# Kernel optimization log

Measured on AMD Instinct MI355X. Metric: run time of the kernel, lower is better.

## Reference

```python
import jax, jax.numpy as jnp
import numpy as np

B, L, D, DIN, S, R, K = 2, 1024, 1024, 2048, 16, 64, 4


def setup_inputs() -> dict:
    key = jax.random.key(0)
    ks = jax.random.split(key, 8)
    f = lambda k, sh, sc: jax.random.normal(k, sh, jnp.float32) * sc
    return {
        "x": f(ks[0], (B, L, D), 1.0),
        "norm_w": jnp.ones((D,), jnp.float32),
        "W_in": f(ks[1], (D, 2 * DIN), D ** -0.5),
        "conv_w": f(ks[2], (DIN, 1, K), 0.5),
        "conv_b": jnp.zeros((DIN,), jnp.float32),
        "W_x": f(ks[3], (DIN, R + 2 * S), DIN ** -0.5),
        "W_dt": f(ks[4], (R, DIN), R ** -0.5),
        "b_dt": f(ks[5], (DIN,), 0.1),
        "A_log": jnp.log(jnp.broadcast_to(jnp.arange(1, S + 1, dtype=jnp.float32), (DIN, S))),
        "D_skip": jnp.ones((DIN,), jnp.float32),
        "W_out": f(ks[6], (DIN, D), DIN ** -0.5),
    }


def reference(x, norm_w, W_in, conv_w, conv_b, W_x, W_dt, b_dt, A_log, D_skip, W_out):
    eps = 1e-5
    # RMSNorm
    xn = x * jax.lax.rsqrt(jnp.mean(x * x, axis=-1, keepdims=True) + eps) * norm_w
    # input projection -> (x_branch, gate)
    xz = xn @ W_in                       # [B,L,2*DIN]
    xi, z = jnp.split(xz, 2, axis=-1)
    # causal depthwise conv1d along L
    xt = jnp.transpose(xi, (0, 2, 1))    # [B,DIN,L]
    xc = jax.lax.conv_general_dilated(xt, conv_w, (1,), [(K - 1, 0)],
                                      feature_group_count=DIN)
    xc = jnp.transpose(xc, (0, 2, 1)) + conv_b
    xc = jax.nn.silu(xc)                 # [B,L,DIN]
    # input-dependent SSM parameters
    xd = xc @ W_x                        # [B,L,R+2S]
    dt, Bm, Cm = jnp.split(xd, [R, R + S], axis=-1)
    dt = jax.nn.softplus(dt @ W_dt + b_dt)           # [B,L,DIN]
    A = -jnp.exp(A_log)                              # [DIN,S]
    dA = jnp.exp(dt[..., None] * A)                  # [B,L,DIN,S]
    dBu = (dt * xc)[..., None] * Bm[:, :, None, :]   # [B,L,DIN,S]
    # selective scan: h_t = dA_t * h_{t-1} + dBu_t (parallel associative scan)
    def comb(c1, c2):
        a1, b1 = c1
        a2, b2 = c2
        return a1 * a2, a2 * b1 + b2
    _, h = jax.lax.associative_scan(comb, (dA, dBu), axis=1)
    y = jnp.einsum('blds,bls->bld', h, Cm) + D_skip * xc
    y = y * jax.nn.silu(z)
    return x + y @ W_out
```

## Files before the change

kernel.cpp:

```cpp
#include <hip/hip_runtime.h>

#define B_    2
#define L_    1024
#define D_    1024
#define DIN_  2048
#define S_    16
#define R_    64
#define NTOK  (B_ * L_)
#define NCH   32
#define LC    (L_ / NCH)

typedef unsigned short u16;
typedef short bf16x8 __attribute__((ext_vector_type(8)));
typedef float f32x4  __attribute__((ext_vector_type(4)));

__device__ __forceinline__ u16 f2bf(float f) {
    union { float f; unsigned u; } v; v.f = f;
    return (u16)((v.u + 0x7FFFu + ((v.u >> 16) & 1u)) >> 16);
}
__device__ __forceinline__ float bf2f(u16 b) {
    union { unsigned u; float f; } v; v.u = (unsigned)b << 16;
    return v.f;
}

__device__ __forceinline__ void transp_tile(
    const float* __restrict__ src, u16* __restrict__ dst,
    int R, int Csrc, int cx, int cy, int tx, int ty) {
    __shared__ float tile[32][33];
    int c0 = cx * 32, r0 = cy * 32;
#pragma unroll
    for (int i = 0; i < 32; i += 8)
        tile[ty + i][tx] = (c0 + tx < Csrc)
            ? src[(size_t)(r0 + ty + i) * Csrc + c0 + tx] : 0.f;
    __syncthreads();
#pragma unroll
    for (int i = 0; i < 32; i += 8)
        dst[(size_t)(c0 + ty + i) * R + r0 + tx] = f2bf(tile[tx][ty + i]);
}

__global__ __launch_bounds__(256) void prep_kernel(
    const float* __restrict__ x, const float* __restrict__ nw, u16* __restrict__ xn,
    const float* __restrict__ W_in,  u16* __restrict__ WinT,
    const float* __restrict__ W_out, u16* __restrict__ WoutT,
    const float* __restrict__ W_x,   u16* __restrict__ WxT,
    const float* __restrict__ W_dt,  u16* __restrict__ WdtT) {
    int bid = blockIdx.x;
    if (bid < NTOK) {
        int row = bid;
        const float4 v = ((const float4*)(x + (size_t)row * D_))[threadIdx.x];
        float ss = v.x * v.x + v.y * v.y + v.z * v.z + v.w * v.w;
#pragma unroll
        for (int o = 32; o > 0; o >>= 1) ss += __shfl_down(ss, o);
        __shared__ float red[4];
        if ((threadIdx.x & 63) == 0) red[threadIdx.x >> 6] = ss;
        __syncthreads();
        float tot = red[0] + red[1] + red[2] + red[3];
        float sc = rsqrtf(tot * (1.f / (float)D_) + 1e-5f);
        const float4 wv = ((const float4*)nw)[threadIdx.x];
        ushort4 o;
        o.x = f2bf(v.x * sc * wv.x);
        o.y = f2bf(v.y * sc * wv.y);
        o.z = f2bf(v.z * sc * wv.z);
        o.w = f2bf(v.w * sc * wv.w);
        ((ushort4*)(xn + (size_t)row * D_))[threadIdx.x] = o;
        return;
    }
    int b2 = bid - NTOK;
    int tx = threadIdx.x & 31, ty = threadIdx.x >> 5;
    if (b2 < 4096) {
        transp_tile(W_in, WinT, D_, 2 * DIN_, b2 % 128, b2 / 128, tx, ty);
    } else if (b2 < 6144) {
        int b = b2 - 4096;
        transp_tile(W_out, WoutT, DIN_, D_, b % 32, b / 32, tx, ty);
    } else if (b2 < 6400) {
        int b = b2 - 6144;
        transp_tile(W_x, WxT, DIN_, 96, b % 4, b / 4, tx, ty);
    } else {
        int b = b2 - 6400;
        transp_tile(W_dt, WdtT, R_, DIN_, b % 64, b / 64, tx, ty);
    }
}

#define BK 32
template<int BM, int BN, int CX>
__global__ __launch_bounds__(256) void gemm_bf16(
    const u16* __restrict__ A, int lda,
    const u16* __restrict__ Bt, int ldb,
    float* __restrict__ C, u16* __restrict__ Cbf, int ldc,
    const float* __restrict__ aux,
    int M, int N, int K, int mode) {
    constexpr int WGM = (BM >= 128) ? 2 : 1;
    constexpr int WGN = 4 / WGM;
    constexpr int FM = BM / (16 * WGM);
    constexpr int FN = BN / (16 * WGN);
    constexpr int ABYTES = BM * BK * 2;
    constexpr int BBYTES = BN * BK * 2;
    __shared__ __align__(16) u16 As[2][BM * BK];
    __shared__ __align__(16) u16 Bs[2][BN * BK];
    const int t = threadIdx.x;
    const int w = t >> 6;
    const int l = t & 63;
    const int lr = l & 15;
    const int kg = l >> 4;
    const int wm = (w / WGN) * (BM / WGM);
    const int wn = (w % WGN) * (BN / WGN);

    const int GX = gridDim.x, GY = gridDim.y;
    int h = blockIdx.x + GX * (blockIdx.y + GY * blockIdx.z);
    int xcd = h & 7, pos = h >> 3;
    int ncx = GX / CX;
    int chunk = (GX * GY * gridDim.z) >> 3;
    int rpc = chunk / CX;
    int bx = (xcd % ncx) * CX + pos % CX;
    int r  = (xcd / ncx) * rpc + pos / CX;
    int by = r % GY;
    int bz = r / GY;

    const int row0 = by * BM;
    const int col0 = bx * BN;
    const int kbase = bz * K;

    auto stage = [&](int buf, int k0) {
#pragma unroll
        for (int i = 0; i < ABYTES; i += 4096) {
            int off = i + t * 16;
            int grow = off >> 6;
            int sw = ((off >> 4) & 3) ^ ((grow >> 1) & 3);
            const u16* ga = A + (size_t)(row0 + grow) * lda + k0 + sw * 8;
            __builtin_amdgcn_global_load_lds(
                (const __attribute__((address_space(1))) unsigned int*)(const void*)ga,
                (__attribute__((address_space(3))) unsigned int*)(void*)&As[buf][off >> 1],
                16, 0, 0);
        }
#pragma unroll
        for (int i = 0; i < BBYTES; i += 4096) {
            int off = i + t * 16;
            int grow = off >> 6;
            int sw = ((off >> 4) & 3) ^ ((grow >> 1) & 3);
            const u16* gb = Bt + (size_t)(col0 + grow) * ldb + k0 + sw * 8;
            __builtin_amdgcn_global_load_lds(
                (const __attribute__((address_space(1))) unsigned int*)(const void*)gb,
                (__attribute__((address_space(3))) unsigned int*)(void*)&Bs[buf][off >> 1],
                16, 0, 0);
        }
    };

    f32x4 acc[FM][FN];
#pragma unroll
    for (int i = 0; i < FM; ++i)
#pragma unroll
        for (int j = 0; j < FN; ++j) acc[i][j] = (f32x4){0.f, 0.f, 0.f, 0.f};

    const int nt = K / BK;
    stage(0, kbase);
    asm volatile("s_waitcnt vmcnt(0)" ::: "memory");
    __builtin_amdgcn_s_barrier();
    asm volatile("" ::: "memory");

    int cur = 0;
    for (int tt = 0; tt < nt; ++tt) {
        if (tt + 1 < nt) stage(cur ^ 1, kbase + (tt + 1) * BK);
        bf16x8 af[FM], bfr[FN];
#pragma unroll
        for (int mt = 0; mt < FM; ++mt) {
            int ar = wm + mt * 16 + lr;
            af[mt] = *(const bf16x8*)&As[cur][ar * 32 + (kg ^ ((ar >> 1) & 3)) * 8];
        }
#pragma unroll
        for (int nt2 = 0; nt2 < FN; ++nt2) {
            int br = wn + nt2 * 16 + lr;
            bfr[nt2] = *(const bf16x8*)&Bs[cur][br * 32 + (kg ^ ((br >> 1) & 3)) * 8];
        }
        __builtin_amdgcn_s_setprio(1);
#pragma unroll
        for (int mt = 0; mt < FM; ++mt)
#pragma unroll
            for (int nt2 = 0; nt2 < FN; ++nt2)
                acc[mt][nt2] = __builtin_amdgcn_mfma_f32_16x16x32_bf16(
                    af[mt], bfr[nt2], acc[mt][nt2], 0, 0, 0);
        __builtin_amdgcn_s_setprio(0);
        if (tt + 1 < nt) {
            asm volatile("s_waitcnt vmcnt(0)" ::: "memory");
            __builtin_amdgcn_s_barrier();
            asm volatile("" ::: "memory");
        }
        cur ^= 1;
    }

    size_t pbase = (mode == 3) ? (size_t)bz * M * N : 0;
#pragma unroll
    for (int mt = 0; mt < FM; ++mt) {
#pragma unroll
        for (int nt2 = 0; nt2 < FN; ++nt2) {
#pragma unroll
            for (int r2 = 0; r2 < 4; ++r2) {
                int row = row0 + wm + mt * 16 + kg * 4 + r2;
                int col = col0 + wn + nt2 * 16 + lr;
                float v = acc[mt][nt2][r2];
                if (mode == 1) { v += aux[col]; v = (v > 20.f) ? v : log1pf(__expf(v)); }
                else if (mode == 2) { v += aux[(size_t)row * ldc + col]; }
                if (C)   C[pbase + (size_t)row * ldc + col] = v;
                if (Cbf) Cbf[pbase + (size_t)row * ldc + col] = f2bf(v);
            }
        }
    }
}

__global__ __launch_bounds__(256) void reduce_wx_kernel(
    const u16* __restrict__ part, float* __restrict__ xd, u16* __restrict__ xdb) {
    int i = blockIdx.x * 256 + threadIdx.x;
    float sx = 0.f, sy = 0.f, sz = 0.f, sw = 0.f;
#pragma unroll
    for (int k = 0; k < 16; ++k) {
        ushort4 v = ((const ushort4*)(part + (size_t)k * NTOK * 128))[i];
        sx += bf2f(v.x); sy += bf2f(v.y); sz += bf2f(v.z); sw += bf2f(v.w);
    }
    float4 s = {sx, sy, sz, sw};
    ((float4*)xd)[i] = s;
    ushort4 o; o.x = f2bf(sx); o.y = f2bf(sy); o.z = f2bf(sz); o.w = f2bf(sw);
    ((ushort4*)xdb)[i] = o;
}

__global__ __launch_bounds__(256) void reduce_out_kernel(
    const u16* __restrict__ part, const float* __restrict__ x, float* __restrict__ out) {
    int i = blockIdx.x * 256 + threadIdx.x;
    float sx = 0.f, sy = 0.f, sz = 0.f, sw = 0.f;
#pragma unroll
    for (int k = 0; k < 4; ++k) {
        ushort4 v = ((const ushort4*)(part + (size_t)k * NTOK * D_))[i];
        sx += bf2f(v.x); sy += bf2f(v.y); sz += bf2f(v.z); sw += bf2f(v.w);
    }
    float4 xv = ((const float4*)x)[i];
    float4 s = {sx + xv.x, sy + xv.y, sz + xv.z, sw + xv.w};
    ((float4*)out)[i] = s;
}

__global__ __launch_bounds__(256) void conv_silu_kernel(
    const u16* __restrict__ xzb, const float* __restrict__ cw,
    const float* __restrict__ cb, u16* __restrict__ xcb) {
    size_t idx = (size_t)blockIdx.x * 256 + threadIdx.x;
    int c = (int)(idx & (DIN_ - 1));
    int g = (int)(idx >> 11);
    int bl0 = g * 4;
    int l0 = bl0 & (L_ - 1);
    const float4 w = ((const float4*)cw)[c];
    float bias = cb[c];
    float v[7];
#pragma unroll
    for (int k = 0; k < 7; ++k) {
        int off = k - 3;
        v[k] = (l0 + off >= 0) ? bf2f(xzb[(size_t)(bl0 + off) * 4096 + c]) : 0.f;
    }
#pragma unroll
    for (int j = 0; j < 4; ++j) {
        float acc = bias + v[j] * w.x + v[j + 1] * w.y + v[j + 2] * w.z + v[j + 3] * w.w;
        float s = acc / (1.f + __expf(-acc));
        xcb[(size_t)(bl0 + j) * DIN_ + c] = f2bf(s);
    }
}

__global__ __launch_bounds__(256) void scan_chunk_kernel(
    const u16* __restrict__ dtq, const u16* __restrict__ xcb,
    const float* __restrict__ xd, const float* __restrict__ A_log,
    float* __restrict__ Pout, float* __restrict__ Hout) {
    int din = blockIdx.x * 256 + threadIdx.x;
    int c = blockIdx.y, b = blockIdx.z;
    float a[S_], h[S_];
#pragma unroll
    for (int q = 0; q < 4; ++q) {
        float4 av = ((const float4*)(A_log + (size_t)din * S_))[q];
        a[q * 4 + 0] = -__expf(av.x); a[q * 4 + 1] = -__expf(av.y);
        a[q * 4 + 2] = -__expf(av.z); a[q * 4 + 3] = -__expf(av.w);
    }
#pragma unroll
    for (int s = 0; s < S_; ++s) h[s] = 0.f;
    float sdt = 0.f;
    size_t rbase = (size_t)b * L_ + (size_t)c * LC;
#pragma unroll 2
    for (int i = 0; i < LC; ++i) {
        size_t row = rbase + i;
        float dtv = bf2f(dtq[row * DIN_ + din]);
        float xcv = bf2f(xcb[row * DIN_ + din]);
        float du = dtv * xcv;
        sdt += dtv;
        const float4* bp = (const float4*)(xd + row * 128 + 64);
        float4 B0 = bp[0], B1 = bp[1], B2 = bp[2], B3 = bp[3];
        float Bv[S_] = {B0.x, B0.y, B0.z, B0.w, B1.x, B1.y, B1.z, B1.w,
                        B2.x, B2.y, B2.z, B2.w, B3.x, B3.y, B3.z, B3.w};
#pragma unroll
        for (int s = 0; s < S_; ++s) {
            float dA = __expf(dtv * a[s]);
            h[s] = h[s] * dA + du * Bv[s];
        }
    }
    size_t obase = ((size_t)(b * NCH + c) * DIN_ + din) * S_;
#pragma unroll
    for (int q = 0; q < 4; ++q) {
        float4 pv, hv;
        pv.x = __expf(a[q * 4 + 0] * sdt); pv.y = __expf(a[q * 4 + 1] * sdt);
        pv.z = __expf(a[q * 4 + 2] * sdt); pv.w = __expf(a[q * 4 + 3] * sdt);
        hv.x = h[q * 4 + 0]; hv.y = h[q * 4 + 1]; hv.z = h[q * 4 + 2]; hv.w = h[q * 4 + 3];
        ((float4*)(Pout + obase))[q] = pv;
        ((float4*)(Hout + obase))[q] = hv;
    }
}

__global__ __launch_bounds__(256) void scan_combine_kernel(
    const float* __restrict__ P, const float* __restrict__ H,
    float* __restrict__ h0) {
    int tid = blockIdx.x * 256 + threadIdx.x;
    int ds = tid & (DIN_ * S_ - 1);
    int b = tid >> 15;
    float h = 0.f;
#pragma unroll
    for (int c = 0; c < NCH; ++c) {
        size_t idx = ((size_t)(b * NCH + c) * DIN_ * S_) + ds;
        h0[idx] = h;
        h = H[idx] + P[idx] * h;
    }
}

__global__ __launch_bounds__(256) void scan_final_kernel(
    const u16* __restrict__ dtq, const u16* __restrict__ xcb,
    const float* __restrict__ xd, const float* __restrict__ A_log,
    const float* __restrict__ h0, const float* __restrict__ Dskip,
    const u16* __restrict__ xzb, u16* __restrict__ yg) {
    int din = blockIdx.x * 256 + threadIdx.x;
    int c = blockIdx.y, b = blockIdx.z;
    float a[S_], h[S_];
#pragma unroll
    for (int q = 0; q < 4; ++q) {
        float4 av = ((const float4*)(A_log + (size_t)din * S_))[q];
        a[q * 4 + 0] = -__expf(av.x); a[q * 4 + 1] = -__expf(av.y);
        a[q * 4 + 2] = -__expf(av.z); a[q * 4 + 3] = -__expf(av.w);
    }
    size_t ibase = ((size_t)(b * NCH + c) * DIN_ + din) * S_;
#pragma unroll
    for (int q = 0; q < 4; ++q) {
        float4 hv = ((const float4*)(h0 + ibase))[q];
        h[q * 4 + 0] = hv.x; h[q * 4 + 1] = hv.y; h[q * 4 + 2] = hv.z; h[q * 4 + 3] = hv.w;
    }
    float dsk = Dskip[din];
    size_t rbase = (size_t)b * L_ + (size_t)c * LC;
#pragma unroll 2
    for (int i = 0; i < LC; ++i) {
        size_t row = rbase + i;
        float dtv = bf2f(dtq[row * DIN_ + din]);
        float xcv = bf2f(xcb[row * DIN_ + din]);
        float du = dtv * xcv;
        const float4* bp = (const float4*)(xd + row * 128 + 64);
        float4 B0 = bp[0], B1 = bp[1], B2 = bp[2], B3 = bp[3];
        const float4* cp = (const float4*)(xd + row * 128 + 80);
        float4 C0 = cp[0], C1 = cp[1], C2 = cp[2], C3 = cp[3];
        float Bv[S_] = {B0.x, B0.y, B0.z, B0.w, B1.x, B1.y, B1.z, B1.w,
                        B2.x, B2.y, B2.z, B2.w, B3.x, B3.y, B3.z, B3.w};
        float Cv[S_] = {C0.x, C0.y, C0.z, C0.w, C1.x, C1.y, C1.z, C1.w,
                        C2.x, C2.y, C2.z, C2.w, C3.x, C3.y, C3.z, C3.w};
        float py = 0.f;
#pragma unroll
        for (int s = 0; s < S_; ++s) {
            float dA = __expf(dtv * a[s]);
            h[s] = h[s] * dA + du * Bv[s];
            py += h[s] * Cv[s];
        }
        float zv = bf2f(xzb[row * 4096 + DIN_ + din]);
        float y = (py + dsk * xcv) * (zv / (1.f + __expf(-zv)));
        yg[row * DIN_ + din] = f2bf(y);
    }
}

extern "C" void kernel_launch(void* const* d_in, const int* in_sizes, int n_in,
                              void* d_out, int out_size, void* d_ws, size_t ws_size,
                              hipStream_t stream) {
    const float* x      = (const float*)d_in[0];
    const float* norm_w = (const float*)d_in[1];
    const float* W_in   = (const float*)d_in[2];
    const float* conv_w = (const float*)d_in[3];
    const float* conv_b = (const float*)d_in[4];
    const float* W_x    = (const float*)d_in[5];
    const float* W_dt   = (const float*)d_in[6];
    const float* b_dt   = (const float*)d_in[7];
    const float* A_log  = (const float*)d_in[8];
    const float* D_skip = (const float*)d_in[9];
    const float* W_out  = (const float*)d_in[10];
    float* out = (float*)d_out;

    char* p = (char*)d_ws;
    auto alloc = [&](size_t bytes) {
        char* r = p;
        p += (bytes + 255) & ~(size_t)255;
        return r;
    };
    u16*   xn      = (u16*)alloc((size_t)NTOK * D_ * 2);
    u16*   WinT    = (u16*)alloc((size_t)2 * DIN_ * D_ * 2);
    u16*   WoutT   = (u16*)alloc((size_t)D_ * DIN_ * 2);
    u16*   WxT     = (u16*)alloc((size_t)128 * DIN_ * 2);
    u16*   WdtT    = (u16*)alloc((size_t)DIN_ * R_ * 2);
    u16*   xzb     = (u16*)alloc((size_t)NTOK * 2 * DIN_ * 2);
    u16*   xcb     = (u16*)alloc((size_t)NTOK * DIN_ * 2);
    float* xd      = (float*)alloc((size_t)NTOK * 128 * 4);
    u16*   xdb     = (u16*)alloc((size_t)NTOK * 128 * 2);
    u16*   dtq     = (u16*)alloc((size_t)NTOK * DIN_ * 2);
    u16*   yg      = (u16*)alloc((size_t)NTOK * DIN_ * 2);
    float* Pbuf    = (float*)alloc((size_t)B_ * NCH * DIN_ * S_ * 4);
    float* Hbuf    = (float*)alloc((size_t)B_ * NCH * DIN_ * S_ * 4);
    float* h0buf   = (float*)alloc((size_t)B_ * NCH * DIN_ * S_ * 4);
    u16*   part_out = (u16*)alloc((size_t)4 * NTOK * D_ * 2);
    u16*   part_wx  = part_out;

    prep_kernel<<<NTOK + 6528, 256, 0, stream>>>(
        x, norm_w, xn, W_in, WinT, W_out, WoutT, W_x, WxT, W_dt, WdtT);

    gemm_bf16<64, 128, 8><<<dim3(2 * DIN_ / 128, NTOK / 64), 256, 0, stream>>>(
        xn, D_, WinT, D_, nullptr, xzb, 2 * DIN_, nullptr, NTOK, 2 * DIN_, D_, 0);
    conv_silu_kernel<<<(NTOK * DIN_ / 4) / 256, 256, 0, stream>>>(xzb, conv_w, conv_b, xcb);
    gemm_bf16<64, 128, 1><<<dim3(1, NTOK / 64, 16), 256, 0, stream>>>(
        xcb, DIN_, WxT, DIN_, nullptr, part_wx, 128, nullptr, NTOK, 128, DIN_ / 16, 3);
    reduce_wx_kernel<<<(NTOK * 128 / 4) / 256, 256, 0, stream>>>(part_wx, xd, xdb);
    gemm_bf16<64, 128, 8><<<dim3(DIN_ / 128, NTOK / 64), 256, 0, stream>>>(
        xdb, 128, WdtT, R_, nullptr, dtq, DIN_, b_dt, NTOK, DIN_, R_, 1);
    {
        dim3 grid(DIN_ / 256, NCH, B_);
        scan_chunk_kernel<<<grid, 256, 0, stream>>>(dtq, xcb, xd, A_log, Pbuf, Hbuf);
        scan_combine_kernel<<<(B_ * DIN_ * S_) / 256, 256, 0, stream>>>(Pbuf, Hbuf, h0buf);
        scan_final_kernel<<<grid, 256, 0, stream>>>(dtq, xcb, xd, A_log, h0buf, D_skip, xzb, yg);
    }
    gemm_bf16<64, 128, 8><<<dim3(D_ / 128, NTOK / 64, 4), 256, 0, stream>>>(
        yg, DIN_, WoutT, DIN_, nullptr, part_out, D_, nullptr, NTOK, D_, DIN_ / 4, 3);
    reduce_out_kernel<<<(NTOK * D_ / 4) / 256, 256, 0, stream>>>(part_out, x, out);
}
```

Measured before the change: 167.8 us.

## Fuse chunked scan, combine and final passes into one kernel with LDS carry

```diff
diff --git a/kernel.cpp b/kernel.cpp
--- a/kernel.cpp
+++ b/kernel.cpp
@@ -259,12 +259,18 @@
     }
 }
 
-__global__ __launch_bounds__(256) void scan_chunk_kernel(
+__global__ __launch_bounds__(256) void scan_fused_kernel(
     const u16* __restrict__ dtq, const u16* __restrict__ xcb,
     const float* __restrict__ xd, const float* __restrict__ A_log,
-    float* __restrict__ Pout, float* __restrict__ Hout) {
-    int din = blockIdx.x * 256 + threadIdx.x;
-    int c = blockIdx.y, b = blockIdx.z;
+    const float* __restrict__ Dskip, const u16* __restrict__ xzb,
+    u16* __restrict__ yg) {
+    __shared__ float Pl[NCH * 8 * S_];
+    __shared__ float Hl[NCH * 8 * S_];
+    const int t = threadIdx.x;
+    const int c = t >> 3, dsub = t & 7;
+    const int din = blockIdx.x * 8 + dsub;
+    const int b = blockIdx.y;
+
     float a[S_], h[S_];
 #pragma unroll
     for (int q = 0; q < 4; ++q) {
@@ -276,6 +282,7 @@
     for (int s = 0; s < S_; ++s) h[s] = 0.f;
     float sdt = 0.f;
     size_t rbase = (size_t)b * L_ + (size_t)c * LC;
+
 #pragma unroll 2
     for (int i = 0; i < LC; ++i) {
         size_t row = rbase + i;
@@ -293,55 +300,30 @@
             h[s] = h[s] * dA + du * Bv[s];
         }
     }
-    size_t obase = ((size_t)(b * NCH + c) * DIN_ + din) * S_;
-#pragma unroll
-    for (int q = 0; q < 4; ++q) {
-        float4 pv, hv;
-        pv.x = __expf(a[q * 4 + 0] * sdt); pv.y = __expf(a[q * 4 + 1] * sdt);
-        pv.z = __expf(a[q * 4 + 2] * sdt); pv.w = __expf(a[q * 4 + 3] * sdt);
-        hv.x = h[q * 4 + 0]; hv.y = h[q * 4 + 1]; hv.z = h[q * 4 + 2]; hv.w = h[q * 4 + 3];
-        ((float4*)(Pout + obase))[q] = pv;
-        ((float4*)(Hout + obase))[q] = hv;
-    }
-}
-
-__global__ __launch_bounds__(256) void scan_combine_kernel(
-    const float* __restrict__ P, const float* __restrict__ H,
-    float* __restrict__ h0) {
-    int tid = blockIdx.x * 256 + threadIdx.x;
-    int ds = tid & (DIN_ * S_ - 1);
-    int b = tid >> 15;
-    float h = 0.f;
-#pragma unroll
-    for (int c = 0; c < NCH; ++c) {
-        size_t idx = ((size_t)(b * NCH + c) * DIN_ * S_) + ds;
-        h0[idx] = h;
-        h = H[idx] + P[idx] * h;
-    }
-}
-
-__global__ __launch_bounds__(256) void scan_final_kernel(
-    const u16* __restrict__ dtq, const u16* __restrict__ xcb,
-    const float* __restrict__ xd, const float* __restrict__ A_log,
-    const float* __restrict__ h0, const float* __restrict__ Dskip,
-    const u16* __restrict__ xzb, u16* __restrict__ yg) {
-    int din = blockIdx.x * 256 + threadIdx.x;
-    int c = blockIdx.y, b = blockIdx.z;
-    float a[S_], h[S_];
-#pragma unroll
-    for (int q = 0; q < 4; ++q) {
-        float4 av = ((const float4*)(A_log + (size_t)din * S_))[q];
-        a[q * 4 + 0] = -__expf(av.x); a[q * 4 + 1] = -__expf(av.y);
-        a[q * 4 + 2] = -__expf(av.z); a[q * 4 + 3] = -__expf(av.w);
-    }
-    size_t ibase = ((size_t)(b * NCH + c) * DIN_ + din) * S_;
-#pragma unroll
-    for (int q = 0; q < 4; ++q) {
-        float4 hv = ((const float4*)(h0 + ibase))[q];
-        h[q * 4 + 0] = hv.x; h[q * 4 + 1] = hv.y; h[q * 4 + 2] = hv.z; h[q * 4 + 3] = hv.w;
-    }
+    const int base = (c * 8 + dsub) * S_;
+#pragma unroll
+    for (int s = 0; s < S_; ++s) {
+        Pl[base + s] = __expf(a[s] * sdt);
+        Hl[base + s] = h[s];
+    }
+    __syncthreads();
+
+    if (t < 8 * S_) {
+        int dsub2 = t & 7, s2 = t >> 3;
+        float hh = 0.f;
+#pragma unroll
+        for (int cc = 0; cc < NCH; ++cc) {
+            int idx = (cc * 8 + dsub2) * S_ + s2;
+            float Pv = Pl[idx], Hv = Hl[idx];
+            Pl[idx] = hh;
+            hh = Hv + Pv * hh;
+        }
+    }
+    __syncthreads();
+
+#pragma unroll
+    for (int s = 0; s < S_; ++s) h[s] = Pl[base + s];
     float dsk = Dskip[din];
-    size_t rbase = (size_t)b * L_ + (size_t)c * LC;
 #pragma unroll 2
     for (int i = 0; i < LC; ++i) {
         size_t row = rbase + i;
@@ -402,9 +384,6 @@
     u16*   xdb     = (u16*)alloc((size_t)NTOK * 128 * 2);
     u16*   dtq     = (u16*)alloc((size_t)NTOK * DIN_ * 2);
     u16*   yg      = (u16*)alloc((size_t)NTOK * DIN_ * 2);
-    float* Pbuf    = (float*)alloc((size_t)B_ * NCH * DIN_ * S_ * 4);
-    float* Hbuf    = (float*)alloc((size_t)B_ * NCH * DIN_ * S_ * 4);
-    float* h0buf   = (float*)alloc((size_t)B_ * NCH * DIN_ * S_ * 4);
     u16*   part_out = (u16*)alloc((size_t)4 * NTOK * D_ * 2);
     u16*   part_wx  = part_out;
 
@@ -419,12 +398,8 @@
     reduce_wx_kernel<<<(NTOK * 128 / 4) / 256, 256, 0, stream>>>(part_wx, xd, xdb);
     gemm_bf16<64, 128, 8><<<dim3(DIN_ / 128, NTOK / 64), 256, 0, stream>>>(
         xdb, 128, WdtT, R_, nullptr, dtq, DIN_, b_dt, NTOK, DIN_, R_, 1);
-    {
-        dim3 grid(DIN_ / 256, NCH, B_);
-        scan_chunk_kernel<<<grid, 256, 0, stream>>>(dtq, xcb, xd, A_log, Pbuf, Hbuf);
-        scan_combine_kernel<<<(B_ * DIN_ * S_) / 256, 256, 0, stream>>>(Pbuf, Hbuf, h0buf);
-        scan_final_kernel<<<grid, 256, 0, stream>>>(dtq, xcb, xd, A_log, h0buf, D_skip, xzb, yg);
-    }
+    scan_fused_kernel<<<dim3(DIN_ / 8, B_), 256, 0, stream>>>(
+        dtq, xcb, xd, A_log, D_skip, xzb, yg);
     gemm_bf16<64, 128, 8><<<dim3(D_ / 128, NTOK / 64, 4), 256, 0, stream>>>(
         yg, DIN_, WoutT, DIN_, nullptr, part_out, D_, nullptr, NTOK, D_, DIN_ / 4, 3);
     reduce_out_kernel<<<(NTOK * D_ / 4) / 256, 256, 0, stream>>>(part_out, x, out);
```

Result: slower. 176.3 us (+5.1%).
